# Kernel tuning notes

Hardware: AMD Instinct MI355X
Metric: run time of the kernel (lower is better)

The kernel has to match this reference:

```python
import jax, jax.numpy as jnp
import numpy as np

N = 50000   # nodes
E = 400000  # edges per relation
R = 3       # relations
IN, HID, C, H = 128, 64, 40, 3  # in_feat, hidden_feat, n_classes, num_heads
NEG_SLOPE = 0.2  # DGL GATConv default leaky_relu slope


def setup_inputs() -> dict:
    key = jax.random.key(0)
    ks = jax.random.split(key, 12)
    feat = jax.random.normal(ks[0], (N, IN), jnp.float32)
    src = jax.random.randint(ks[1], (R, E), 0, N, dtype=jnp.int32)
    dst = jax.random.randint(ks[2], (R, E), 0, N, dtype=jnp.int32)

    def w(k, shape, fan):
        return jax.random.normal(k, shape, jnp.float32) / np.float32(np.sqrt(fan))

    # layer 1: in_feat -> hidden_feat, relu activation
    W1 = w(ks[3], (R, IN, H * HID), IN)
    al1 = w(ks[4], (R, H, HID), HID)
    ar1 = w(ks[5], (R, H, HID), HID)
    b1 = jnp.zeros((R, H * HID), jnp.float32)
    # layer 2: hidden_feat -> n_classes, no activation
    W2 = w(ks[6], (R, HID, H * C), HID)
    al2 = w(ks[7], (R, H, C), C)
    ar2 = w(ks[8], (R, H, C), C)
    b2 = jnp.zeros((R, H * C), jnp.float32)
    return dict(feat=feat, src=src, dst=dst, W1=W1, al1=al1, ar1=ar1, b1=b1,
                W2=W2, al2=al2, ar2=ar2, b2=b2)


def gat_hetero_layer(feat, src, dst, W, al, ar, b, apply_relu):
    """HeteroGraphConv(mean) over R relations, each a GATConv + head-mean."""
    n = feat.shape[0]

    def one_relation(src_r, dst_r, W_r, al_r, ar_r, b_r):
        n_heads, out = al_r.shape
        z = (feat @ W_r).reshape(n, n_heads, out)          # [N,H,out]
        el = jnp.sum(z * al_r, axis=-1)                    # [N,H]
        er = jnp.sum(z * ar_r, axis=-1)                    # [N,H]
        e = jax.nn.leaky_relu(el[src_r] + er[dst_r], NEG_SLOPE)  # [E,H]
        # edge softmax over incoming edges of each dst node
        m = jax.ops.segment_max(e, dst_r, num_segments=n)  # [N,H]
        a = jnp.exp(e - m[dst_r])                          # [E,H]
        s = jax.ops.segment_sum(a, dst_r, num_segments=n)  # [N,H]
        alpha = a / s[dst_r]                               # [E,H]
        msg = alpha[:, :, None] * z[src_r]                 # [E,H,out]
        rst = jax.ops.segment_sum(msg, dst_r, num_segments=n)  # [N,H,out]
        rst = rst + b_r.reshape(n_heads, out)
        if apply_relu:
            rst = jax.nn.relu(rst)
        return rst.mean(axis=1)                            # head mean -> [N,out]

    outs = jax.vmap(one_relation)(src, dst, W, al, ar, b)  # [R,N,out]
    return outs.mean(axis=0)                               # relation mean


def reference(feat, src, dst, W1, al1, ar1, b1, W2, al2, ar2, b2):
    h = gat_hetero_layer(feat, src, dst, W1, al1, ar1, b1, True)
    h = gat_hetero_layer(h, src, dst, W2, al2, ar2, b2, False)
    return h
```

## Files before the change

### kernel.cpp

```cpp
#include <hip/hip_runtime.h>

#define R_   3
#define N_   50000
#define E_   400000
#define IN_  128
#define HID_ 64
#define C_   40
#define H_   3
#define NEG_SLOPE 0.2f
#define LOG2E 1.4426950408889634f

#define SCAN_CHUNK 1024
#define NCH  49
#define NCH2 64

#define MPAD 50048
#define NRT  3128

typedef _Float16 half_t;
typedef _Float16 f16x8 __attribute__((ext_vector_type(8)));
typedef _Float16 f16x4 __attribute__((ext_vector_type(4)));
typedef float float4v __attribute__((ext_vector_type(4)));

template <int V> struct vecT;
template <> struct vecT<4> { typedef f16x4 type; };
template <> struct vecT<8> { typedef f16x8 type; };

__global__ void zero_kernel(float* __restrict__ p, size_t n) {
    size_t i = (size_t)blockIdx.x * blockDim.x + threadIdx.x;
    if (i < n) p[i] = 0.f;
}

__global__ void cast_tiled_kernel(const float* __restrict__ feat, half_t* __restrict__ At) {
    int idx = blockIdx.x * 256 + threadIdx.x;
    const int TOT = NRT * 4 * 64;
    if (idx >= TOT) return;
    int lane = idx & 63;
    int kb = (idx >> 6) & 3;
    int rowtile = idx >> 8;
    int row = rowtile * 16 + (lane & 15);
    int k = kb * 32 + (lane >> 4) * 8;
    f16x8 h = {};
    if (row < N_) {
        const float* p = feat + (size_t)row * IN_ + k;
        float4 a = ((const float4*)p)[0];
        float4 b = ((const float4*)p)[1];
        h[0] = (half_t)a.x; h[1] = (half_t)a.y; h[2] = (half_t)a.z; h[3] = (half_t)a.w;
        h[4] = (half_t)b.x; h[5] = (half_t)b.y; h[6] = (half_t)b.z; h[7] = (half_t)b.w;
    }
    ((f16x8*)At)[idx] = h;
}

template <int K, int NY>
__global__ void bprep_kernel(const float* __restrict__ W, half_t* __restrict__ Bf, int Nc) {
    constexpr int KB = K / 32;
    int idx = blockIdx.x * 256 + threadIdx.x;
    const int TOT = R_ * NY * KB * 4 * 64;
    if (idx >= TOT) return;
    int lane = idx & 63;
    int ct = (idx >> 6) & 3;
    int t = idx >> 8;
    int kb = t % KB; t /= KB;
    int y = t % NY;  int r = t / NY;
    int col = y * 64 + ct * 16 + (lane & 15);
    int k0 = kb * 32 + (lane >> 4) * 8;
    f16x8 h = {};
    if (col < Nc) {
        #pragma unroll
        for (int j = 0; j < 8; ++j)
            h[j] = (half_t)W[((size_t)r * K + k0 + j) * Nc + col];
    }
    ((f16x8*)Bf)[idx] = h;
}

__global__ void hist_kernel(const int* __restrict__ dst, int* __restrict__ deg) {
    int idx = blockIdx.x * 256 + threadIdx.x;
    if (idx < R_ * E_) {
        int r = idx / E_;
        atomicAdd(&deg[r * N_ + dst[idx]], 1);
    }
}

__global__ void scanA_kernel(const int* __restrict__ deg, int* __restrict__ bsum) {
    int r = blockIdx.y, ch = blockIdx.x, tid = threadIdx.x;
    int base = ch * SCAN_CHUNK + tid * 4;
    int s = 0;
    for (int j = 0; j < 4; ++j) {
        int i = base + j;
        if (i < N_) s += deg[r * N_ + i];
    }
    __shared__ int red[256];
    red[tid] = s; __syncthreads();
    for (int off = 128; off; off >>= 1) {
        if (tid < off) red[tid] += red[tid + off];
        __syncthreads();
    }
    if (tid == 0) bsum[r * NCH2 + ch] = red[0];
}

__global__ void scanB_kernel(int* __restrict__ bsum) {
    int w = threadIdx.x >> 6;
    int l = threadIdx.x & 63;
    if (w < R_) {
        int v = (l < NCH) ? bsum[w * NCH2 + l] : 0;
        int s = v;
        #pragma unroll
        for (int off = 1; off < 64; off <<= 1) {
            int t = __shfl_up(s, off);
            if (l >= off) s += t;
        }
        if (l < NCH) bsum[w * NCH2 + l] = s - v;
    }
}

__global__ void scanC_kernel(const int* __restrict__ deg, const int* __restrict__ bsum,
                             int* __restrict__ rowptr, int* __restrict__ cursor) {
    int r = blockIdx.y, ch = blockIdx.x, tid = threadIdx.x;
    int base = ch * SCAN_CHUNK + tid * 4;
    int v[4]; int s = 0;
    for (int j = 0; j < 4; ++j) {
        int i = base + j;
        v[j] = (i < N_) ? deg[r * N_ + i] : 0;
        s += v[j];
    }
    __shared__ int buf[256];
    buf[tid] = s; __syncthreads();
    for (int off = 1; off < 256; off <<= 1) {
        int t2 = (tid >= off) ? buf[tid - off] : 0;
        __syncthreads();
        buf[tid] += t2;
        __syncthreads();
    }
    int excl = buf[tid] - s + bsum[r * NCH2 + ch];
    int run = excl;
    for (int j = 0; j < 4; ++j) {
        int i = base + j;
        if (i < N_) {
            rowptr[r * (N_ + 1) + i] = run;
            cursor[r * N_ + i] = run;
            run += v[j];
        }
    }
    if (ch == 0 && tid == 0) rowptr[r * (N_ + 1) + N_] = E_;
}

__global__ void fill_kernel(const int* __restrict__ src, const int* __restrict__ dst,
                            int* __restrict__ cursor, int* __restrict__ csr_src) {
    int idx = blockIdx.x * 256 + threadIdx.x;
    if (idx < R_ * E_) {
        int r = idx / E_;
        int pos = atomicAdd(&cursor[r * N_ + dst[idx]], 1);
        csr_src[(size_t)r * E_ + pos] = src[idx] * 3;
    }
}

template <int K, int NY, bool FUSE>
__global__ __launch_bounds__(256) void mfma_gemm3_kernel(
        const half_t* __restrict__ At, const half_t* __restrict__ Bf,
        half_t* __restrict__ Z, int Nc,
        const float* __restrict__ al, const float* __restrict__ ar,
        float* __restrict__ el, float* __restrict__ er) {
    constexpr int KB = K / 32;
    int r = blockIdx.z, y = blockIdx.y;
    int wave = threadIdx.x >> 6, lane = threadIdx.x & 63;
    int rowtile = blockIdx.x * 4 + wave;
    const f16x8* Ap = (const f16x8*)At + (size_t)rowtile * KB * 64 + lane;
    const f16x8* Bp = (const f16x8*)Bf + (size_t)(r * NY + y) * KB * 4 * 64 + lane;
    float4v acc[4] = {};
    #pragma unroll
    for (int kb = 0; kb < KB; ++kb) {
        f16x8 af = Ap[kb * 64];
        #pragma unroll
        for (int ct = 0; ct < 4; ++ct) {
            f16x8 bf = Bp[(kb * 4 + ct) * 64];
            acc[ct] = __builtin_amdgcn_mfma_f32_16x16x32_f16(af, bf, acc[ct], 0, 0, 0);
        }
    }
    int lrow = lane & 15, lq = lane >> 4;
    half_t* Zr = Z + (size_t)r * N_ * Nc;
    int rbase = rowtile * 16 + lq * 4;
    int col0 = y * 64;
    float elv[4] = {}, erv[4] = {};
    const float* alp;
    const float* arp;
    if constexpr (FUSE) {
        alp = al + ((size_t)r * H_ + y) * 64;
        arp = ar + ((size_t)r * H_ + y) * 64;
    }
    #pragma unroll
    for (int ct = 0; ct < 4; ++ct) {
        int col = col0 + ct * 16 + lrow;
        if (col >= Nc) continue;
        float wa = 0.f, wb = 0.f;
        if constexpr (FUSE) { wa = alp[ct * 16 + lrow]; wb = arp[ct * 16 + lrow]; }
        #pragma unroll
        for (int g = 0; g < 4; ++g) {
            int row = rbase + g;
            half_t zh = (half_t)acc[ct][g];
            if (row < N_) Zr[(size_t)row * Nc + col] = zh;
            if constexpr (FUSE) {
                float zf = (float)zh;
                elv[g] = fmaf(zf, wa, elv[g]);
                erv[g] = fmaf(zf, wb, erv[g]);
            }
        }
    }
    if constexpr (FUSE) {
        #pragma unroll
        for (int g = 0; g < 4; ++g) {
            #pragma unroll
            for (int m = 1; m < 16; m <<= 1) {
                elv[g] += __shfl_xor(elv[g], m);
                erv[g] += __shfl_xor(erv[g], m);
            }
        }
        if (lrow == 0) {
            #pragma unroll
            for (int g = 0; g < 4; ++g) {
                int row = rbase + g;
                if (row < N_) {
                    size_t o = ((size_t)r * N_ + row) * H_ + y;
                    el[o] = elv[g] * LOG2E;
                    er[o] = erv[g] * LOG2E;
                }
            }
        }
    }
}

template <int Dd>
__global__ __launch_bounds__(256) void attn2_kernel(
        const half_t* __restrict__ z, const float* __restrict__ al,
        const float* __restrict__ ar, float* __restrict__ el,
        float* __restrict__ er) {
    int t = blockIdx.x * 256 + threadIdx.x;
    if (t >= R_ * N_ * H_) return;
    int rn = t / H_, h = t - rn * H_;
    int r = rn / N_;
    const half_t* zrow = z + (size_t)rn * (3 * Dd) + h * Dd;
    const float* alp = al + (r * H_ + h) * Dd;
    const float* arp = ar + (r * H_ + h) * Dd;
    float p0 = 0.f, p1 = 0.f, q0 = 0.f, q1 = 0.f;
    #pragma unroll
    for (int c = 0; c < Dd / 8; ++c) {
        f16x8 zv = *(const f16x8*)(zrow + c * 8);
        #pragma unroll
        for (int j = 0; j < 8; j += 2) {
            float za = (float)zv[j], zb = (float)zv[j + 1];
            p0 += za * alp[c * 8 + j];
            p1 += zb * alp[c * 8 + j + 1];
            q0 += za * arp[c * 8 + j];
            q1 += zb * arp[c * 8 + j + 1];
        }
    }
    el[t] = (p0 + p1) * LOG2E;
    er[t] = (q0 + q1) * LOG2E;
}

template <int Dd, int VEC, bool RELU, typename OutT, bool TILED>
__global__ __launch_bounds__(256) void agg14_kernel(
        const int* __restrict__ rowptr, const int* __restrict__ csr_src,
        const half_t* __restrict__ z, const float* __restrict__ el,
        const float* __restrict__ er, const float* __restrict__ bias,
        OutT* __restrict__ out, float scale) {
    constexpr int ROWH = 3 * Dd;
    constexpr int LPE  = ROWH / VEC;
    constexpr int PH   = Dd / VEC;
    using fv = typename vecT<VEC>::type;
    int n = blockIdx.x * 4 + (threadIdx.x >> 6);
    int lane = threadIdx.x & 63;
    if (n >= N_) return;
    int hf = lane >> 5;
    int sub = lane & 31;
    bool act = sub < LPE;
    int hl = act ? sub / PH : 0;
    int dl = act ? sub - hl * PH : 0;
    int zoff = VEC * sub;
    int ii[R_], ee[R_];
    float ervv[R_];
    #pragma unroll
    for (int r = 0; r < R_; ++r) {
        ii[r] = rowptr[r * (N_ + 1) + n];
        ee[r] = rowptr[r * (N_ + 1) + n + 1];
        ervv[r] = er[((size_t)r * N_ + n) * H_ + hl];
    }
    fv ah[R_] = {};
    float ll[R_] = {};
    while (ii[0] < ee[0] || ii[1] < ee[1] || ii[2] < ee[2]) {
        fv zA[R_], zB[R_];
        float xA[R_], xB[R_];
        bool okA[R_], okB[R_];
        #pragma unroll
        for (int r = 0; r < R_; ++r) {
            const int* cs = csr_src + (size_t)r * E_;
            const half_t* zr = z + (size_t)r * N_ * ROWH;
            const float* elr = el + (size_t)r * N_ * H_;
            int eA = ii[r] + hf, eB = ii[r] + 2 + hf;
            okA[r] = eA < ee[r];
            okB[r] = eB < ee[r];
            int sA = cs[okA[r] ? eA : 0];
            int sB = cs[okB[r] ? eB : 0];
            xA[r] = elr[sA + hl] + ervv[r];
            xB[r] = elr[sB + hl] + ervv[r];
            zA[r] = {}; zB[r] = {};
            if (act) {
                zA[r] = *(const fv*)(zr + (size_t)sA * Dd + zoff);
                zB[r] = *(const fv*)(zr + (size_t)sB * Dd + zoff);
            }
        }
        #pragma unroll
        for (int r = 0; r < R_; ++r) {
            float xa = xA[r]; xa = fmaxf(xa, NEG_SLOPE * xa);
            float xb = xB[r]; xb = fmaxf(xb, NEG_SLOPE * xb);
            float cA = okA[r] ? __builtin_amdgcn_exp2f(xa) : 0.f;
            float cB = okB[r] ? __builtin_amdgcn_exp2f(xb) : 0.f;
            ll[r] += cA + cB;
            half_t hA = (half_t)cA, hB = (half_t)cB;
            fv vA, vB;
            #pragma unroll
            for (int v = 0; v < VEC; ++v) { vA[v] = hA; vB[v] = hB; }
            ah[r] += vA * zA[r] + vB * zB[r];
        }
        #pragma unroll
        for (int r = 0; r < R_; ++r) ii[r] += 4;
    }
    float aa[R_][VEC];
    #pragma unroll
    for (int r = 0; r < R_; ++r)
        #pragma unroll
        for (int v = 0; v < VEC; ++v) aa[r][v] = (float)ah[r][v];
    #pragma unroll
    for (int r = 0; r < R_; ++r) {
        #pragma unroll
        for (int v = 0; v < VEC; ++v) aa[r][v] += __shfl(aa[r][v], lane ^ 32);
        ll[r] += __shfl(ll[r], lane ^ 32);
    }
    float vacc[VEC] = {};
    #pragma unroll
    for (int r = 0; r < R_; ++r) {
        float li = (ll[r] > 0.f) ? 1.f / ll[r] : 0.f;
        const float* br = bias + r * ROWH + hl * Dd + VEC * dl;
        #pragma unroll
        for (int v = 0; v < VEC; ++v) {
            float t = aa[r][v] * li + br[v];
            if (RELU) t = fmaxf(t, 0.f);
            vacc[v] += t;
        }
    }
    int base = lane & 32;
    int p1 = sub + PH;     if (p1 >= LPE) p1 -= LPE;
    int p2 = sub + 2 * PH; if (p2 >= LPE) p2 -= LPE;
    #pragma unroll
    for (int v = 0; v < VEC; ++v)
        vacc[v] += __shfl(vacc[v], base + p1) + __shfl(vacc[v], base + p2);
    int srcl = lane / VEC;
    int cm = lane & (VEC - 1);
    float tv[VEC];
    #pragma unroll
    for (int v = 0; v < VEC; ++v) tv[v] = __shfl(vacc[v], srcl);
    float outv = tv[0];
    #pragma unroll
    for (int v = 1; v < VEC; ++v) outv = (cm == v) ? tv[v] : outv;
    if constexpr (TILED) {
        int rowtile = n >> 4;
        int kb = lane >> 5;
        int fl = (n & 15) + ((lane >> 3) & 3) * 16;
        int elo = lane & 7;
        size_t ho = (((size_t)rowtile * 2 + kb) * 64 + fl) * 8 + elo;
        ((half_t*)out)[ho] = (half_t)(outv * scale);
    } else {
        if (lane < Dd) out[(size_t)n * Dd + lane] = (OutT)(outv * scale);
    }
}

static inline size_t align256(size_t x) { return (x + 255) & ~(size_t)255; }

extern "C" void kernel_launch(void* const* d_in, const int* in_sizes, int n_in,
                              void* d_out, int out_size, void* d_ws, size_t ws_size,
                              hipStream_t stream) {
    const float* feat = (const float*)d_in[0];
    const int*   src  = (const int*)d_in[1];
    const int*   dst  = (const int*)d_in[2];
    const float* W1   = (const float*)d_in[3];
    const float* al1  = (const float*)d_in[4];
    const float* ar1  = (const float*)d_in[5];
    const float* b1   = (const float*)d_in[6];
    const float* W2   = (const float*)d_in[7];
    const float* al2  = (const float*)d_in[8];
    const float* ar2  = (const float*)d_in[9];
    const float* b2   = (const float*)d_in[10];
    float* out = (float*)d_out;

    char* ws = (char*)d_ws;
    size_t off = 0;
    half_t* zbuf  = (half_t*)(ws + off); off += align256((size_t)R_ * N_ * (3 * HID_) * 2);
    half_t* featT = (half_t*)(ws + off); off += align256((size_t)NRT * 4 * 64 * 8 * 2);
    half_t* h1T   = (half_t*)(ws + off); off += align256((size_t)NRT * 2 * 64 * 8 * 2);
    half_t* B1f   = (half_t*)(ws + off); off += align256((size_t)R_ * 3 * 4 * 4 * 64 * 8 * 2);
    half_t* B2f   = (half_t*)(ws + off); off += align256((size_t)R_ * 2 * 2 * 4 * 64 * 8 * 2);
    float* el   = (float*)(ws + off); off += align256((size_t)R_ * N_ * H_ * 4);
    float* er   = (float*)(ws + off); off += align256((size_t)R_ * N_ * H_ * 4);
    int* deg    = (int*)(ws + off);   off += align256((size_t)R_ * N_ * 4);
    int* rowptr = (int*)(ws + off);   off += align256((size_t)R_ * (N_ + 1) * 4);
    int* cursor = (int*)(ws + off);   off += align256((size_t)R_ * N_ * 4);
    int* bsum   = (int*)(ws + off);   off += align256((size_t)R_ * NCH2 * 4);
    int* csr    = (int*)(ws + off);   off += align256((size_t)R_ * E_ * 4);
    (void)ws_size; (void)n_in; (void)in_sizes; (void)out_size;

    const int EDGE_BLOCKS = (R_ * E_ + 255) / 256;
    const int ROW_TILES = (N_ + 63) / 64;
    const int NODE_BLOCKS = (R_ * N_ + 255) / 256;
    const int NODE_WAVES = (N_ + 3) / 4;
    const int ATTN_BLOCKS = (R_ * N_ * H_ + 255) / 256;

    cast_tiled_kernel<<<(NRT * 4 * 64 + 255) / 256, 256, 0, stream>>>(feat, featT);
    bprep_kernel<IN_, 3><<<(R_ * 3 * 4 * 4 * 64 + 255) / 256, 256, 0, stream>>>(W1, B1f, H_ * HID_);
    bprep_kernel<HID_, 2><<<(R_ * 2 * 2 * 4 * 64 + 255) / 256, 256, 0, stream>>>(W2, B2f, H_ * C_);
    zero_kernel<<<7, 256, 0, stream>>>((float*)(h1T + (size_t)3125 * 2 * 512), 1536);

    zero_kernel<<<NODE_BLOCKS, 256, 0, stream>>>((float*)deg, (size_t)R_ * N_);
    hist_kernel<<<EDGE_BLOCKS, 256, 0, stream>>>(dst, deg);
    scanA_kernel<<<dim3(NCH, R_), 256, 0, stream>>>(deg, bsum);
    scanB_kernel<<<1, 192, 0, stream>>>(bsum);
    scanC_kernel<<<dim3(NCH, R_), 256, 0, stream>>>(deg, bsum, rowptr, cursor);
    fill_kernel<<<EDGE_BLOCKS, 256, 0, stream>>>(src, dst, cursor, csr);

    mfma_gemm3_kernel<IN_, 3, true><<<dim3(ROW_TILES, 3, R_), 256, 0, stream>>>(
        featT, B1f, zbuf, H_ * HID_, al1, ar1, el, er);
    agg14_kernel<HID_, 8, true, half_t, true><<<NODE_WAVES, 256, 0, stream>>>(
        rowptr, csr, zbuf, el, er, b1, h1T, 1.f / (H_ * R_));

    mfma_gemm3_kernel<HID_, 2, false><<<dim3(ROW_TILES, 2, R_), 256, 0, stream>>>(
        h1T, B2f, zbuf, H_ * C_, nullptr, nullptr, nullptr, nullptr);
    attn2_kernel<C_><<<ATTN_BLOCKS, 256, 0, stream>>>(zbuf, al2, ar2, el, er);
    agg14_kernel<C_, 4, false, float, false><<<NODE_WAVES, 256, 0, stream>>>(
        rowptr, csr, zbuf, el, er, b2, out, 1.f / (H_ * R_));
}
```

Before: 449.9 us.

## Fuse preprocessing kernels into one launch and fold scanB into scanC

Merges the feature cast, both weight repacks, the h1T pad zeroing and the degree histogram into a single block-range-dispatched prep kernel, and replaces the degree zero kernel with hipMemsetAsync. The block-offset scan is now recomputed by one wave in each scanC block, which removes the separate scanB launch. The histogram and CSR fill now process four edges per thread with their atomics issued back-to-back, to expose more memory-level parallelism. The aim is to cut kernel launch gaps and serialization in the graph-preprocessing stage, at the cost of redundant tiny scans and a more heterogeneous fused kernel.

```diff
diff --git a/kernel.cpp b/kernel.cpp
--- a/kernel.cpp
+++ b/kernel.cpp
@@ -26,35 +26,11 @@
 template <> struct vecT<4> { typedef f16x4 type; };
 template <> struct vecT<8> { typedef f16x8 type; };
 
-__global__ void zero_kernel(float* __restrict__ p, size_t n) {
-    size_t i = (size_t)blockIdx.x * blockDim.x + threadIdx.x;
-    if (i < n) p[i] = 0.f;
-}
-
-__global__ void cast_tiled_kernel(const float* __restrict__ feat, half_t* __restrict__ At) {
-    int idx = blockIdx.x * 256 + threadIdx.x;
-    const int TOT = NRT * 4 * 64;
-    if (idx >= TOT) return;
-    int lane = idx & 63;
-    int kb = (idx >> 6) & 3;
-    int rowtile = idx >> 8;
-    int row = rowtile * 16 + (lane & 15);
-    int k = kb * 32 + (lane >> 4) * 8;
-    f16x8 h = {};
-    if (row < N_) {
-        const float* p = feat + (size_t)row * IN_ + k;
-        float4 a = ((const float4*)p)[0];
-        float4 b = ((const float4*)p)[1];
-        h[0] = (half_t)a.x; h[1] = (half_t)a.y; h[2] = (half_t)a.z; h[3] = (half_t)a.w;
-        h[4] = (half_t)b.x; h[5] = (half_t)b.y; h[6] = (half_t)b.z; h[7] = (half_t)b.w;
-    }
-    ((f16x8*)At)[idx] = h;
-}
 
 template <int K, int NY>
-__global__ void bprep_kernel(const float* __restrict__ W, half_t* __restrict__ Bf, int Nc) {
+__device__ inline void bprep_body(int idx, const float* __restrict__ W,
+                                  half_t* __restrict__ Bf, int Nc) {
     constexpr int KB = K / 32;
-    int idx = blockIdx.x * 256 + threadIdx.x;
     const int TOT = R_ * NY * KB * 4 * 64;
     if (idx >= TOT) return;
     int lane = idx & 63;
@@ -73,11 +49,46 @@
     ((f16x8*)Bf)[idx] = h;
 }
 
-__global__ void hist_kernel(const int* __restrict__ dst, int* __restrict__ deg) {
-    int idx = blockIdx.x * 256 + threadIdx.x;
-    if (idx < R_ * E_) {
-        int r = idx / E_;
-        atomicAdd(&deg[r * N_ + dst[idx]], 1);
+__global__ void prep_kernel(const float* __restrict__ feat, half_t* __restrict__ At,
+                            const float* __restrict__ W1, half_t* __restrict__ B1f,
+                            const float* __restrict__ W2, half_t* __restrict__ B2f,
+                            half_t* __restrict__ h1T,
+                            const int* __restrict__ dst, int* __restrict__ deg) {
+    int b = blockIdx.x;
+    if (b < 3128) {
+        int idx = b * 256 + threadIdx.x;
+        int lane = idx & 63;
+        int kb = (idx >> 6) & 3;
+        int rowtile = idx >> 8;
+        int row = rowtile * 16 + (lane & 15);
+        int k = kb * 32 + (lane >> 4) * 8;
+        f16x8 h = {};
+        if (row < N_) {
+            const float* p = feat + (size_t)row * IN_ + k;
+            float4 a = ((const float4*)p)[0];
+            float4 c = ((const float4*)p)[1];
+            h[0] = (half_t)a.x; h[1] = (half_t)a.y; h[2] = (half_t)a.z; h[3] = (half_t)a.w;
+            h[4] = (half_t)c.x; h[5] = (half_t)c.y; h[6] = (half_t)c.z; h[7] = (half_t)c.w;
+        }
+        ((f16x8*)At)[idx] = h;
+    } else if (b < 3164) {
+        bprep_body<IN_, 3>((b - 3128) * 256 + threadIdx.x, W1, B1f, H_ * HID_);
+    } else if (b < 3176) {
+        bprep_body<HID_, 2>((b - 3164) * 256 + threadIdx.x, W2, B2f, H_ * C_);
+    } else if (b < 3188) {
+        int i = (b - 3176) * 256 + threadIdx.x;
+        if (i < 3072) h1T[(size_t)3125 * 2 * 512 + i] = (half_t)0.f;
+    } else {
+        const int T = (R_ * E_) / 4;
+        int t = (b - 3188) * 256 + threadIdx.x;
+        if (t < T) {
+            #pragma unroll
+            for (int j = 0; j < 4; ++j) {
+                int idx = t + j * T;
+                int r = idx / E_;
+                atomicAdd(&deg[r * N_ + dst[idx]], 1);
+            }
+        }
     }
 }
 
@@ -98,24 +109,20 @@
     if (tid == 0) bsum[r * NCH2 + ch] = red[0];
 }
 
-__global__ void scanB_kernel(int* __restrict__ bsum) {
-    int w = threadIdx.x >> 6;
-    int l = threadIdx.x & 63;
-    if (w < R_) {
-        int v = (l < NCH) ? bsum[w * NCH2 + l] : 0;
-        int s = v;
-        #pragma unroll
-        for (int off = 1; off < 64; off <<= 1) {
-            int t = __shfl_up(s, off);
-            if (l >= off) s += t;
-        }
-        if (l < NCH) bsum[w * NCH2 + l] = s - v;
-    }
-}
-
 __global__ void scanC_kernel(const int* __restrict__ deg, const int* __restrict__ bsum,
                              int* __restrict__ rowptr, int* __restrict__ cursor) {
     int r = blockIdx.y, ch = blockIdx.x, tid = threadIdx.x;
+    __shared__ int chbase_s;
+    if (tid < 64) {
+        int v = (tid < NCH) ? bsum[r * NCH2 + tid] : 0;
+        int s = v;
+        #pragma unroll
+        for (int off = 1; off < 64; off <<= 1) {
+            int t = __shfl_up(s, off);
+            if (tid >= off) s += t;
+        }
+        if (tid == ch) chbase_s = s - v;
+    }
     int base = ch * SCAN_CHUNK + tid * 4;
     int v[4]; int s = 0;
     for (int j = 0; j < 4; ++j) {
@@ -131,7 +138,7 @@
         buf[tid] += t2;
         __syncthreads();
     }
-    int excl = buf[tid] - s + bsum[r * NCH2 + ch];
+    int excl = buf[tid] - s + chbase_s;
     int run = excl;
     for (int j = 0; j < 4; ++j) {
         int i = base + j;
@@ -146,12 +153,20 @@
 
 __global__ void fill_kernel(const int* __restrict__ src, const int* __restrict__ dst,
                             int* __restrict__ cursor, int* __restrict__ csr_src) {
-    int idx = blockIdx.x * 256 + threadIdx.x;
-    if (idx < R_ * E_) {
-        int r = idx / E_;
-        int pos = atomicAdd(&cursor[r * N_ + dst[idx]], 1);
-        csr_src[(size_t)r * E_ + pos] = src[idx] * 3;
-    }
+    const int T = (R_ * E_) / 4;
+    int t = blockIdx.x * 256 + threadIdx.x;
+    if (t >= T) return;
+    int pos[4], s3[4], rr[4];
+    #pragma unroll
+    for (int j = 0; j < 4; ++j) {
+        int idx = t + j * T;
+        rr[j] = idx / E_;
+        pos[j] = atomicAdd(&cursor[rr[j] * N_ + dst[idx]], 1);
+        s3[j] = src[idx] * 3;
+    }
+    #pragma unroll
+    for (int j = 0; j < 4; ++j)
+        csr_src[(size_t)rr[j] * E_ + pos[j]] = s3[j];
 }
 
 template <int K, int NY, bool FUSE>
@@ -407,23 +422,19 @@
     int* csr    = (int*)(ws + off);   off += align256((size_t)R_ * E_ * 4);
     (void)ws_size; (void)n_in; (void)in_sizes; (void)out_size;
 
-    const int EDGE_BLOCKS = (R_ * E_ + 255) / 256;
     const int ROW_TILES = (N_ + 63) / 64;
-    const int NODE_BLOCKS = (R_ * N_ + 255) / 256;
     const int NODE_WAVES = (N_ + 3) / 4;
     const int ATTN_BLOCKS = (R_ * N_ * H_ + 255) / 256;
-
-    cast_tiled_kernel<<<(NRT * 4 * 64 + 255) / 256, 256, 0, stream>>>(feat, featT);
-    bprep_kernel<IN_, 3><<<(R_ * 3 * 4 * 4 * 64 + 255) / 256, 256, 0, stream>>>(W1, B1f, H_ * HID_);
-    bprep_kernel<HID_, 2><<<(R_ * 2 * 2 * 4 * 64 + 255) / 256, 256, 0, stream>>>(W2, B2f, H_ * C_);
-    zero_kernel<<<7, 256, 0, stream>>>((float*)(h1T + (size_t)3125 * 2 * 512), 1536);
-
-    zero_kernel<<<NODE_BLOCKS, 256, 0, stream>>>((float*)deg, (size_t)R_ * N_);
-    hist_kernel<<<EDGE_BLOCKS, 256, 0, stream>>>(dst, deg);
+    const int E4_BLOCKS = (R_ * E_ / 4 + 255) / 256;
+    const int PREP_BLOCKS = 3188 + E4_BLOCKS;
+
+    hipMemsetAsync(deg, 0, (size_t)R_ * N_ * 4, stream);
+    prep_kernel<<<PREP_BLOCKS, 256, 0, stream>>>(feat, featT, W1, B1f, W2, B2f,
+                                                 h1T, dst, deg);
+
     scanA_kernel<<<dim3(NCH, R_), 256, 0, stream>>>(deg, bsum);
-    scanB_kernel<<<1, 192, 0, stream>>>(bsum);
     scanC_kernel<<<dim3(NCH, R_), 256, 0, stream>>>(deg, bsum, rowptr, cursor);
-    fill_kernel<<<EDGE_BLOCKS, 256, 0, stream>>>(src, dst, cursor, csr);
+    fill_kernel<<<E4_BLOCKS, 256, 0, stream>>>(src, dst, cursor, csr);
 
     mfma_gemm3_kernel<IN_, 3, true><<<dim3(ROW_TILES, 3, R_), 256, 0, stream>>>(
         featT, B1f, zbuf, H_ * HID_, al1, ar1, el, er);
```

Measured after the change: 441.7 us. Within noise of the previous version (-1.8%).
